# Performance work log

Measured on AMD Instinct MI355X. Metric: run time of the kernel, lower is better.

The kernel has to match this reference:

```python
import jax, jax.numpy as jnp
import numpy as np

H = 12      # num_heads
DIN = 768   # input_embedding_dim
D = 64      # embedding_dim (per head)
N, T = 4, 1024


def setup_inputs() -> dict:
    key = jax.random.key(0)
    ks = jax.random.split(key, 6)
    s_in = 1.0 / np.sqrt(DIN)
    s_hd = 1.0 / np.sqrt(H * D)
    x = jax.random.normal(ks[0], (N, T, DIN), dtype=jnp.float32)
    # Per-head bias-free projections stacked over heads: [H, DIN, D]
    Wq = jax.random.uniform(ks[1], (H, DIN, D), jnp.float32, -s_in, s_in)
    Wk = jax.random.uniform(ks[2], (H, DIN, D), jnp.float32, -s_in, s_in)
    Wv = jax.random.uniform(ks[3], (H, DIN, D), jnp.float32, -s_in, s_in)
    # Output projection: Linear(H*D -> D) with bias
    Wo = jax.random.uniform(ks[4], (H * D, D), jnp.float32, -s_hd, s_hd)
    bo = jax.random.uniform(ks[5], (D,), jnp.float32, -s_hd, s_hd)
    return {"x": x, "Wq": Wq, "Wk": Wk, "Wv": Wv, "Wo": Wo, "bo": bo}


def reference(x, Wq, Wk, Wv, Wo, bo):
    n, t, _ = x.shape
    # Batched per-head projections (all heads at once): [N,H,T,D]
    q = jnp.einsum('ntd,hde->nhte', x, Wq)
    k = jnp.einsum('ntd,hde->nhte', x, Wk)
    v = jnp.einsum('ntd,hde->nhte', x, Wv)
    # Raw scores (note: original applies NO 1/sqrt(D) scaling): [N,H,T,T]
    att = jnp.einsum('nhte,nhse->nhts', q, k)
    # Faithful to torch: tril zeros the upper triangle, then ALL zeros -> -inf
    causal = jnp.tril(jnp.ones((t, t), dtype=bool))
    att = jnp.where(causal, att, 0.0)
    att = jnp.where(att == 0.0, -jnp.inf, att)
    attn = jax.nn.softmax(att, axis=-1)  # [N,H,T,T]
    # Weighted values, then concat heads along feature dim (head-major order)
    o = jnp.einsum('nhts,nhse->nhte', attn, v)          # [N,H,T,D]
    o = jnp.transpose(o, (0, 2, 1, 3)).reshape(n, t, -1)  # [N,T,H*D]
    out = o @ Wo + bo  # [N,T,D]
    return out, attn
```

## Files before the change

### kernel.cpp

```cpp
#include <hip/hip_runtime.h>
#include <hip/hip_bf16.h>

typedef __hip_bfloat16 bf16;
typedef __attribute__((ext_vector_type(8))) short bf16x8;
typedef __attribute__((ext_vector_type(4))) float f32x4;

constexpr int NB  = 4;
constexpr int NH  = 12;
constexpr int SEQ = 1024;
constexpr int HD  = 64;
constexpr int DM  = 768;
constexpr int LDA = 40;

__device__ __forceinline__ bf16x8 ld8(const bf16* p){ return *(const bf16x8*)p; }
__device__ __forceinline__ f32x4 mfma16(bf16x8 a, bf16x8 b, f32x4 c){
  return __builtin_amdgcn_mfma_f32_16x16x32_bf16(a, b, c, 0, 0, 0);
}
union U8 { bf16x8 v; bf16 h[8]; };

__global__ __launch_bounds__(256) void wprep(const float* __restrict__ Wq, const float* __restrict__ Wk,
                      const float* __restrict__ Wv, const float* __restrict__ Wo,
                      bf16* __restrict__ WqTh, bf16* __restrict__ WqTl,
                      bf16* __restrict__ WkTh, bf16* __restrict__ WkTl,
                      bf16* __restrict__ WvT,  bf16* __restrict__ WoT){
  __shared__ float sT[64][65];
  const int tid = threadIdx.x;
  const int dt = blockIdx.x, y = blockIdx.y;
  const float* src; bf16* dh; bf16* dl = nullptr;
  if (y < 36){
    int z = y / 12, h = y % 12;
    src = (z==0 ? Wq : z==1 ? Wk : Wv) + (size_t)h*DM*HD;
    dh  = (z==0 ? WqTh : z==1 ? WkTh : WvT) + (size_t)h*HD*DM;
    if (z==0) dl = WqTl + (size_t)h*HD*DM;
    if (z==1) dl = WkTl + (size_t)h*HD*DM;
  } else { src = Wo; dh = WoT; }

  {
    int r = tid >> 2, c = (tid & 3) * 16;
    const float* sp = src + ((size_t)(dt*64 + r))*HD + c;
    f32x4 v0 = *(const f32x4*)sp, v1 = *(const f32x4*)(sp+4),
          v2 = *(const f32x4*)(sp+8), v3 = *(const f32x4*)(sp+12);
    #pragma unroll
    for (int j = 0; j < 4; j++){
      sT[r][c+j] = v0[j]; sT[r][c+4+j] = v1[j]; sT[r][c+8+j] = v2[j]; sT[r][c+12+j] = v3[j];
    }
  }
  __syncthreads();
  {
    int e = tid >> 2, co = (tid & 3) * 16;
    U8 uh0, ul0, uh1, ul1;
    #pragma unroll
    for (int j = 0; j < 8; j++){
      float v = sT[co + j][e];
      bf16 hi = __float2bfloat16(v);
      uh0.h[j] = hi; ul0.h[j] = __float2bfloat16(v - __bfloat162float(hi));
    }
    #pragma unroll
    for (int j = 0; j < 8; j++){
      float v = sT[co + 8 + j][e];
      bf16 hi = __float2bfloat16(v);
      uh1.h[j] = hi; ul1.h[j] = __float2bfloat16(v - __bfloat162float(hi));
    }
    size_t o = (size_t)e*DM + dt*64 + co;
    *(bf16x8*)(dh + o) = uh0.v; *(bf16x8*)(dh + o + 8) = uh1.v;
    if (dl){ *(bf16x8*)(dl + o) = ul0.v; *(bf16x8*)(dl + o + 8) = ul1.v; }
  }
}

__global__ __launch_bounds__(256) void xprep(const float* __restrict__ x,
                                             bf16* __restrict__ xh, bf16* __restrict__ xl){
  size_t base = ((size_t)blockIdx.x*256 + threadIdx.x)*8;
  f32x4 a = *(const f32x4*)(x + base), b = *(const f32x4*)(x + base + 4);
  U8 uh, ul;
  #pragma unroll
  for (int j = 0; j < 4; j++){
    bf16 h0 = __float2bfloat16(a[j]);
    uh.h[j] = h0; ul.h[j] = __float2bfloat16(a[j] - __bfloat162float(h0));
    bf16 h1 = __float2bfloat16(b[j]);
    uh.h[4+j] = h1; ul.h[4+j] = __float2bfloat16(b[j] - __bfloat162float(h1));
  }
  *(bf16x8*)(xh + base) = uh.v;
  *(bf16x8*)(xl + base) = ul.v;
}

__global__ __launch_bounds__(256) void kproj(const bf16* __restrict__ xh, const bf16* __restrict__ xl,
    const bf16* __restrict__ WqTh, const bf16* __restrict__ WqTl,
    const bf16* __restrict__ WkTh, const bf16* __restrict__ WkTl,
    const bf16* __restrict__ WvT,
    bf16* __restrict__ Qhi, bf16* __restrict__ Qlo,
    bf16* __restrict__ Khi, bf16* __restrict__ Klo, bf16* __restrict__ Vt){
  __shared__ bf16 sA[2][128*LDA];
  __shared__ bf16 sB[4][64*LDA];
  const int tid = threadIdx.x;
  const int lane = tid & 63, w = tid >> 6;
  const int quad = lane >> 4, lc = lane & 15;
  const int mb = blockIdx.x, h = blockIdx.y, z = blockIdx.z;
  const int sr = tid >> 2;
  const int sc = (tid & 3) * 8;
  const int wm = w & 1, wn = w >> 1;

  if (z == 0){
    const bf16* Bqh = WqTh + (size_t)h*HD*DM;
    const bf16* Bql = WqTl + (size_t)h*HD*DM;
    const bf16* Bkh = WkTh + (size_t)h*HD*DM;
    const bf16* Bkl = WkTl + (size_t)h*HD*DM;
    f32x4 aq[4][2] = {}, ak[4][2] = {};
    bf16x8 pa0,pa1,pa2,pa3,pq0,pq1,pk0,pk1;
    auto ldchunk = [&](int kc){
      size_t col = (size_t)kc*32 + sc;
      pa0 = ld8(xh + (size_t)(mb*128 + sr)*DM + col);
      pa1 = ld8(xh + (size_t)(mb*128 + sr + 64)*DM + col);
      pa2 = ld8(xl + (size_t)(mb*128 + sr)*DM + col);
      pa3 = ld8(xl + (size_t)(mb*128 + sr + 64)*DM + col);
      pq0 = ld8(Bqh + (size_t)sr*DM + col);
      pq1 = ld8(Bql + (size_t)sr*DM + col);
      pk0 = ld8(Bkh + (size_t)sr*DM + col);
      pk1 = ld8(Bkl + (size_t)sr*DM + col);
    };
    ldchunk(0);
    for (int kc = 0; kc < DM/32; kc++){
      *(bf16x8*)&sA[0][sr*LDA + sc] = pa0;
      *(bf16x8*)&sA[0][(sr+64)*LDA + sc] = pa1;
      *(bf16x8*)&sA[1][sr*LDA + sc] = pa2;
      *(bf16x8*)&sA[1][(sr+64)*LDA + sc] = pa3;
      *(bf16x8*)&sB[0][sr*LDA + sc] = pq0;
      *(bf16x8*)&sB[1][sr*LDA + sc] = pq1;
      *(bf16x8*)&sB[2][sr*LDA + sc] = pk0;
      *(bf16x8*)&sB[3][sr*LDA + sc] = pk1;
      __syncthreads();
      if (kc < DM/32 - 1) ldchunk(kc + 1);
      bf16x8 bqh[2], bql[2], bkh[2], bkl[2];
      #pragma unroll
      for (int nt = 0; nt < 2; nt++){
        int ro = (wn*32 + nt*16 + lc)*LDA + quad*8;
        bqh[nt] = *(const bf16x8*)&sB[0][ro];
        bql[nt] = *(const bf16x8*)&sB[1][ro];
        bkh[nt] = *(const bf16x8*)&sB[2][ro];
        bkl[nt] = *(const bf16x8*)&sB[3][ro];
      }
      #pragma unroll
      for (int mt = 0; mt < 4; mt++){
        bf16x8 ah = *(const bf16x8*)&sA[0][(wm*64 + mt*16 + lc)*LDA + quad*8];
        bf16x8 al = *(const bf16x8*)&sA[1][(wm*64 + mt*16 + lc)*LDA + quad*8];
        #pragma unroll
        for (int nt = 0; nt < 2; nt++){
          aq[mt][nt] = mfma16(ah, bqh[nt], aq[mt][nt]);
          aq[mt][nt] = mfma16(ah, bql[nt], aq[mt][nt]);
          aq[mt][nt] = mfma16(al, bqh[nt], aq[mt][nt]);
          ak[mt][nt] = mfma16(ah, bkh[nt], ak[mt][nt]);
          ak[mt][nt] = mfma16(ah, bkl[nt], ak[mt][nt]);
          ak[mt][nt] = mfma16(al, bkh[nt], ak[mt][nt]);
        }
      }
      __syncthreads();
    }
    #pragma unroll
    for (int mt = 0; mt < 4; mt++){
      #pragma unroll
      for (int nt = 0; nt < 2; nt++){
        #pragma unroll
        for (int i = 0; i < 4; i++){
          int tg = mb*128 + wm*64 + mt*16 + quad*4 + i;
          int e  = wn*32 + nt*16 + lc;
          int n = tg >> 10, t = tg & 1023;
          size_t o = ((size_t)(n*NH + h)*SEQ + t)*HD + e;
          float vq = aq[mt][nt][i];
          bf16 hq = __float2bfloat16(vq);
          Qhi[o] = hq;
          Qlo[o] = __float2bfloat16(vq - __bfloat162float(hq));
          float vk = ak[mt][nt][i];
          bf16 hk = __float2bfloat16(vk);
          Khi[o] = hk;
          Klo[o] = __float2bfloat16(vk - __bfloat162float(hk));
        }
      }
    }
  } else {
    const bf16* Av = WvT + (size_t)h*HD*DM;
    f32x4 acc[2][4] = {};
    bf16x8 pa0, pb0, pb1;
    auto ldchunk = [&](int kc){
      size_t col = (size_t)kc*32 + sc;
      pa0 = ld8(Av + (size_t)sr*DM + col);
      pb0 = ld8(xh + (size_t)(mb*128 + sr)*DM + col);
      pb1 = ld8(xh + (size_t)(mb*128 + sr + 64)*DM + col);
    };
    ldchunk(0);
    for (int kc = 0; kc < DM/32; kc++){
      *(bf16x8*)&sB[0][sr*LDA + sc] = pa0;
      *(bf16x8*)&sA[0][sr*LDA + sc] = pb0;
      *(bf16x8*)&sA[0][(sr+64)*LDA + sc] = pb1;
      __syncthreads();
      if (kc < DM/32 - 1) ldchunk(kc + 1);
      bf16x8 bt[4];
      #pragma unroll
      for (int nt = 0; nt < 4; nt++)
        bt[nt] = *(const bf16x8*)&sA[0][(wn*64 + nt*16 + lc)*LDA + quad*8];
      #pragma unroll
      for (int mt = 0; mt < 2; mt++){
        bf16x8 a = *(const bf16x8*)&sB[0][(wm*32 + mt*16 + lc)*LDA + quad*8];
        #pragma unroll
        for (int nt = 0; nt < 4; nt++)
          acc[mt][nt] = mfma16(a, bt[nt], acc[mt][nt]);
      }
      __syncthreads();
    }
    #pragma unroll
    for (int mt = 0; mt < 2; mt++){
      #pragma unroll
      for (int nt = 0; nt < 4; nt++){
        #pragma unroll
        for (int i = 0; i < 4; i++){
          int e  = wm*32 + mt*16 + quad*4 + i;
          int tg = mb*128 + wn*64 + nt*16 + lc;
          int n = tg >> 10, t = tg & 1023;
          Vt[((size_t)(n*NH + h)*HD + e)*SEQ + t] = __float2bfloat16(acc[mt][nt][i]);
        }
      }
    }
  }
}

__global__ __launch_bounds__(256) void kattn_pv(const bf16* __restrict__ Qhi, const bf16* __restrict__ Qlo,
                                                const bf16* __restrict__ Khi, const bf16* __restrict__ Klo,
                                                const bf16* __restrict__ Vt,
                                                float* __restrict__ attn, bf16* __restrict__ O){
  __shared__ bf16 sP[16][SEQ + 8];
  __shared__ float msh[4][16], lsh[4][16];
  const int tid = threadIdx.x;
  const int lane = tid & 63, w = tid >> 6;
  const int quad = lane >> 4, lc = lane & 15;
  const int t0 = blockIdx.x * 16;
  const int nh = blockIdx.y;
  const size_t base = (size_t)nh * SEQ * HD;
  const float NEGINF = -__builtin_inff();

  f32x4 acc[16] = {};
  const bf16* qh = Qhi + base + (size_t)(t0 + lc)*HD;
  const bf16* ql = Qlo + base + (size_t)(t0 + lc)*HD;
  bf16x8 ah0 = ld8(qh + quad*8), ah1 = ld8(qh + 32 + quad*8);
  bf16x8 al0 = ld8(ql + quad*8), al1 = ld8(ql + 32 + quad*8);
  const int tmax = t0 + 15;
  const int cbase = w*256;

  bf16x8 kb[2][4];
  auto loadK = [&](int tl, int b){
    const bf16* kh = Khi + base + (size_t)(cbase + tl*16 + lc)*HD;
    const bf16* kl = Klo + base + (size_t)(cbase + tl*16 + lc)*HD;
    kb[b][0] = ld8(kh + quad*8);  kb[b][1] = ld8(kh + 32 + quad*8);
    kb[b][2] = ld8(kl + quad*8);  kb[b][3] = ld8(kl + 32 + quad*8);
  };
  if (cbase <= tmax) loadK(0, 0);
  #pragma unroll
  for (int tl = 0; tl < 16; tl++){
    if (cbase + tl*16 <= tmax){
      if (tl < 15 && cbase + (tl+1)*16 <= tmax) loadK(tl+1, (tl+1)&1);
      const int b = tl & 1;
      acc[tl] = mfma16(ah0, kb[b][0], acc[tl]);
      acc[tl] = mfma16(ah1, kb[b][1], acc[tl]);
      acc[tl] = mfma16(ah0, kb[b][2], acc[tl]);
      acc[tl] = mfma16(ah1, kb[b][3], acc[tl]);
      acc[tl] = mfma16(al0, kb[b][0], acc[tl]);
      acc[tl] = mfma16(al1, kb[b][1], acc[tl]);
    }
  }

  float mx[4] = {NEGINF, NEGINF, NEGINF, NEGINF};
  #pragma unroll
  for (int tl = 0; tl < 16; tl++){
    int col = cbase + tl*16 + lc;
    #pragma unroll
    for (int i = 0; i < 4; i++){
      int r = t0 + quad*4 + i;
      float v = acc[tl][i];
      if (col <= r && v != 0.0f) mx[i] = fmaxf(mx[i], v);
    }
  }
  #pragma unroll
  for (int off = 8; off; off >>= 1){
    #pragma unroll
    for (int i = 0; i < 4; i++) mx[i] = fmaxf(mx[i], __shfl_xor(mx[i], off, 16));
  }
  float sm[4] = {0.f, 0.f, 0.f, 0.f};
  #pragma unroll
  for (int tl = 0; tl < 16; tl++){
    int col = cbase + tl*16 + lc;
    #pragma unroll
    for (int i = 0; i < 4; i++){
      int r = t0 + quad*4 + i;
      float v = acc[tl][i];
      float e = (col <= r && v != 0.0f) ? __expf(v - mx[i]) : 0.0f;
      acc[tl][i] = e;
      sm[i] += e;
    }
  }
  #pragma unroll
  for (int off = 8; off; off >>= 1){
    #pragma unroll
    for (int i = 0; i < 4; i++) sm[i] += __shfl_xor(sm[i], off, 16);
  }
  if (lc == 0){
    #pragma unroll
    for (int i = 0; i < 4; i++){ msh[w][quad*4 + i] = mx[i]; lsh[w][quad*4 + i] = sm[i]; }
  }
  __syncthreads();
  float scale[4];
  #pragma unroll
  for (int i = 0; i < 4; i++){
    int rl = quad*4 + i;
    float M = fmaxf(fmaxf(msh[0][rl], msh[1][rl]), fmaxf(msh[2][rl], msh[3][rl]));
    float L = 0.f;
    #pragma unroll
    for (int w2 = 0; w2 < 4; w2++) L += lsh[w2][rl] * __expf(msh[w2][rl] - M);
    scale[i] = __expf(mx[i] - M) / L;
  }
  #pragma unroll
  for (int tl = 0; tl < 16; tl++){
    int col = cbase + tl*16 + lc;
    #pragma unroll
    for (int i = 0; i < 4; i++){
      sP[quad*4 + i][col] = __float2bfloat16(acc[tl][i] * scale[i]);
    }
  }
  __syncthreads();

  #pragma unroll
  for (int r = 0; r < 16; r++){
    const unsigned* sPu = (const unsigned*)&sP[r][0];
    uint2 v = *(const uint2*)(sPu + tid*2);
    f32x4 f;
    f[0] = __uint_as_float(v.x << 16);
    f[1] = __uint_as_float(v.x & 0xFFFF0000u);
    f[2] = __uint_as_float(v.y << 16);
    f[3] = __uint_as_float(v.y & 0xFFFF0000u);
    *(f32x4*)(attn + ((size_t)nh*SEQ + t0 + r)*SEQ + tid*4) = f;
  }

  f32x4 oacc = {};
  const bf16* Vb = Vt + ((size_t)nh*HD + w*16 + lc)*SEQ;
  const int kend = t0 + 16;
  for (int s0 = 0; s0 < kend; s0 += 32){
    bf16x8 a = *(const bf16x8*)&sP[lc][s0 + quad*8];
    bf16x8 b = ld8(Vb + s0 + quad*8);
    oacc = mfma16(a, b, oacc);
  }
  const int n = nh / NH, h = nh % NH;
  #pragma unroll
  for (int i = 0; i < 4; i++){
    O[((size_t)n*SEQ + t0 + quad*4 + i)*DM + h*HD + w*16 + lc] = __float2bfloat16(oacc[i]);
  }
}

__global__ __launch_bounds__(256) void kout(const bf16* __restrict__ O, const bf16* __restrict__ WoT,
                                            const float* __restrict__ bo, float* __restrict__ out){
  const int lane = threadIdx.x & 63, w = threadIdx.x >> 6;
  const int quad = lane >> 4, lc = lane & 15;
  const int wm = w & 1, wn = w >> 1;
  const int g = blockIdx.x * 32;
  const int n = g >> 10, tb = g & 1023;
  const bf16* Or = O + ((size_t)n*SEQ + tb + wm*16 + lc)*DM;
  f32x4 acc[2] = {};
  for (int k0 = 0; k0 < DM; k0 += 32){
    bf16x8 a = ld8(Or + k0 + quad*8);
    #pragma unroll
    for (int nt = 0; nt < 2; nt++){
      bf16x8 b = ld8(WoT + (size_t)(wn*32 + nt*16 + lc)*DM + k0 + quad*8);
      acc[nt] = mfma16(a, b, acc[nt]);
    }
  }
  #pragma unroll
  for (int nt = 0; nt < 2; nt++){
    float bias = bo[wn*32 + nt*16 + lc];
    #pragma unroll
    for (int i = 0; i < 4; i++){
      out[((size_t)n*SEQ + tb + wm*16 + quad*4 + i)*HD + wn*32 + nt*16 + lc] = acc[nt][i] + bias;
    }
  }
}

extern "C" void kernel_launch(void* const* d_in, const int* in_sizes, int n_in,
                              void* d_out, int out_size, void* d_ws, size_t ws_size,
                              hipStream_t stream){
  const float* x  = (const float*)d_in[0];
  const float* Wq = (const float*)d_in[1];
  const float* Wk = (const float*)d_in[2];
  const float* Wv = (const float*)d_in[3];
  const float* Wo = (const float*)d_in[4];
  const float* bo = (const float*)d_in[5];

  float* out  = (float*)d_out;
  float* attn = out + (size_t)NB*SEQ*HD;

  constexpr size_t SZ_WT  = (size_t)NH*HD*DM;
  constexpr size_t SZ_WOT = (size_t)HD*DM;
  constexpr size_t SZ_Q   = (size_t)NB*NH*SEQ*HD;
  bf16* b = (bf16*)d_ws;
  bf16* WqTh = b;  b += SZ_WT;
  bf16* WqTl = b;  b += SZ_WT;
  bf16* WkTh = b;  b += SZ_WT;
  bf16* WkTl = b;  b += SZ_WT;
  bf16* WvT  = b;  b += SZ_WT;
  bf16* WoT  = b;  b += SZ_WOT;
  bf16* xh   = b;  b += SZ_Q;
  bf16* xl   = b;  b += SZ_Q;
  bf16* Qhi  = b;  b += SZ_Q;
  bf16* Qlo  = b;  b += SZ_Q;
  bf16* Khi  = b;  b += SZ_Q;
  bf16* Klo  = b;  b += SZ_Q;
  bf16* Vt   = b;  b += SZ_Q;
  bf16* O    = xh;

  wprep<<<dim3(12, 37), 256, 0, stream>>>(Wq, Wk, Wv, Wo, WqTh, WqTl, WkTh, WkTl, WvT, WoT);
  xprep<<<dim3((int)(SZ_Q/(256*8))), 256, 0, stream>>>(x, xh, xl);
  kproj<<<dim3(NB*SEQ/128, NH, 2), 256, 0, stream>>>(xh, xl, WqTh, WqTl, WkTh, WkTl, WvT,
                                                     Qhi, Qlo, Khi, Klo, Vt);
  kattn_pv<<<dim3(SEQ/16, NB*NH), 256, 0, stream>>>(Qhi, Qlo, Khi, Klo, Vt, attn, O);
  kout<<<dim3(NB*SEQ/32), 256, 0, stream>>>(O, WoT, bo, out);
}
```

Measured before the change: 361.0 us.

## Fuse V projection into QK projection blocks and drop softmax max pass

The projection kernel now computes Q, K and V in one block per row-tile, so x is loaded once for all three; V is transposed through shared memory and written with vector stores. The attention kernel drops the row-max pass and exponentiates raw scores directly, which removes a reduction, a shared-memory exchange and extra exps, but risks overflow if scores are large. It also removes K double-buffering and moves the PV matmul ahead of the attn store. The V projection now runs with fewer blocks, and the missing max subtraction only holds while raw scores stay small enough for exp.

```diff
diff --git a/kernel.cpp b/kernel.cpp
--- a/kernel.cpp
+++ b/kernel.cpp
@@ -11,6 +11,7 @@
 constexpr int HD  = 64;
 constexpr int DM  = 768;
 constexpr int LDA = 40;
+constexpr int LDV = 138;
 
 __device__ __forceinline__ bf16x8 ld8(const bf16* p){ return *(const bf16x8*)p; }
 __device__ __forceinline__ f32x4 mfma16(bf16x8 a, bf16x8 b, f32x4 c){
@@ -90,133 +91,121 @@
     bf16* __restrict__ Qhi, bf16* __restrict__ Qlo,
     bf16* __restrict__ Khi, bf16* __restrict__ Klo, bf16* __restrict__ Vt){
   __shared__ bf16 sA[2][128*LDA];
-  __shared__ bf16 sB[4][64*LDA];
+  __shared__ bf16 sB[5][64*LDA];
   const int tid = threadIdx.x;
   const int lane = tid & 63, w = tid >> 6;
   const int quad = lane >> 4, lc = lane & 15;
-  const int mb = blockIdx.x, h = blockIdx.y, z = blockIdx.z;
+  const int mb = blockIdx.x, h = blockIdx.y;
   const int sr = tid >> 2;
   const int sc = (tid & 3) * 8;
   const int wm = w & 1, wn = w >> 1;
 
-  if (z == 0){
-    const bf16* Bqh = WqTh + (size_t)h*HD*DM;
-    const bf16* Bql = WqTl + (size_t)h*HD*DM;
-    const bf16* Bkh = WkTh + (size_t)h*HD*DM;
-    const bf16* Bkl = WkTl + (size_t)h*HD*DM;
-    f32x4 aq[4][2] = {}, ak[4][2] = {};
-    bf16x8 pa0,pa1,pa2,pa3,pq0,pq1,pk0,pk1;
-    auto ldchunk = [&](int kc){
-      size_t col = (size_t)kc*32 + sc;
-      pa0 = ld8(xh + (size_t)(mb*128 + sr)*DM + col);
-      pa1 = ld8(xh + (size_t)(mb*128 + sr + 64)*DM + col);
-      pa2 = ld8(xl + (size_t)(mb*128 + sr)*DM + col);
-      pa3 = ld8(xl + (size_t)(mb*128 + sr + 64)*DM + col);
-      pq0 = ld8(Bqh + (size_t)sr*DM + col);
-      pq1 = ld8(Bql + (size_t)sr*DM + col);
-      pk0 = ld8(Bkh + (size_t)sr*DM + col);
-      pk1 = ld8(Bkl + (size_t)sr*DM + col);
-    };
-    ldchunk(0);
-    for (int kc = 0; kc < DM/32; kc++){
-      *(bf16x8*)&sA[0][sr*LDA + sc] = pa0;
-      *(bf16x8*)&sA[0][(sr+64)*LDA + sc] = pa1;
-      *(bf16x8*)&sA[1][sr*LDA + sc] = pa2;
-      *(bf16x8*)&sA[1][(sr+64)*LDA + sc] = pa3;
-      *(bf16x8*)&sB[0][sr*LDA + sc] = pq0;
-      *(bf16x8*)&sB[1][sr*LDA + sc] = pq1;
-      *(bf16x8*)&sB[2][sr*LDA + sc] = pk0;
-      *(bf16x8*)&sB[3][sr*LDA + sc] = pk1;
-      __syncthreads();
-      if (kc < DM/32 - 1) ldchunk(kc + 1);
-      bf16x8 bqh[2], bql[2], bkh[2], bkl[2];
+  const bf16* Bqh = WqTh + (size_t)h*HD*DM;
+  const bf16* Bql = WqTl + (size_t)h*HD*DM;
+  const bf16* Bkh = WkTh + (size_t)h*HD*DM;
+  const bf16* Bkl = WkTl + (size_t)h*HD*DM;
+  const bf16* Bv  = WvT  + (size_t)h*HD*DM;
+
+  f32x4 aq[4][2] = {}, ak[4][2] = {}, av[4][2] = {};
+  bf16x8 pa0,pa1,pa2,pa3,pq0,pq1,pk0,pk1,pv0;
+  auto ldchunk = [&](int kc){
+    size_t col = (size_t)kc*32 + sc;
+    pa0 = ld8(xh + (size_t)(mb*128 + sr)*DM + col);
+    pa1 = ld8(xh + (size_t)(mb*128 + sr + 64)*DM + col);
+    pa2 = ld8(xl + (size_t)(mb*128 + sr)*DM + col);
+    pa3 = ld8(xl + (size_t)(mb*128 + sr + 64)*DM + col);
+    pq0 = ld8(Bqh + (size_t)sr*DM + col);
+    pq1 = ld8(Bql + (size_t)sr*DM + col);
+    pk0 = ld8(Bkh + (size_t)sr*DM + col);
+    pk1 = ld8(Bkl + (size_t)sr*DM + col);
+    pv0 = ld8(Bv  + (size_t)sr*DM + col);
+  };
+  ldchunk(0);
+  for (int kc = 0; kc < DM/32; kc++){
+    *(bf16x8*)&sA[0][sr*LDA + sc] = pa0;
+    *(bf16x8*)&sA[0][(sr+64)*LDA + sc] = pa1;
+    *(bf16x8*)&sA[1][sr*LDA + sc] = pa2;
+    *(bf16x8*)&sA[1][(sr+64)*LDA + sc] = pa3;
+    *(bf16x8*)&sB[0][sr*LDA + sc] = pq0;
+    *(bf16x8*)&sB[1][sr*LDA + sc] = pq1;
+    *(bf16x8*)&sB[2][sr*LDA + sc] = pk0;
+    *(bf16x8*)&sB[3][sr*LDA + sc] = pk1;
+    *(bf16x8*)&sB[4][sr*LDA + sc] = pv0;
+    __syncthreads();
+    if (kc < DM/32 - 1) ldchunk(kc + 1);
+    bf16x8 bqh[2], bql[2], bkh[2], bkl[2], bv[2];
+    #pragma unroll
+    for (int nt = 0; nt < 2; nt++){
+      int ro = (wn*32 + nt*16 + lc)*LDA + quad*8;
+      bqh[nt] = *(const bf16x8*)&sB[0][ro];
+      bql[nt] = *(const bf16x8*)&sB[1][ro];
+      bkh[nt] = *(const bf16x8*)&sB[2][ro];
+      bkl[nt] = *(const bf16x8*)&sB[3][ro];
+      bv[nt]  = *(const bf16x8*)&sB[4][ro];
+    }
+    #pragma unroll
+    for (int mt = 0; mt < 4; mt++){
+      bf16x8 ah = *(const bf16x8*)&sA[0][(wm*64 + mt*16 + lc)*LDA + quad*8];
+      bf16x8 al = *(const bf16x8*)&sA[1][(wm*64 + mt*16 + lc)*LDA + quad*8];
       #pragma unroll
       for (int nt = 0; nt < 2; nt++){
-        int ro = (wn*32 + nt*16 + lc)*LDA + quad*8;
-        bqh[nt] = *(const bf16x8*)&sB[0][ro];
-        bql[nt] = *(const bf16x8*)&sB[1][ro];
-        bkh[nt] = *(const bf16x8*)&sB[2][ro];
-        bkl[nt] = *(const bf16x8*)&sB[3][ro];
+        aq[mt][nt] = mfma16(ah, bqh[nt], aq[mt][nt]);
+        aq[mt][nt] = mfma16(ah, bql[nt], aq[mt][nt]);
+        aq[mt][nt] = mfma16(al, bqh[nt], aq[mt][nt]);
+        ak[mt][nt] = mfma16(ah, bkh[nt], ak[mt][nt]);
+        ak[mt][nt] = mfma16(ah, bkl[nt], ak[mt][nt]);
+        ak[mt][nt] = mfma16(al, bkh[nt], ak[mt][nt]);
+        av[mt][nt] = mfma16(ah, bv[nt],  av[mt][nt]);
       }
+    }
+    __syncthreads();
+  }
+
+  const int nA = mb >> 3, tbase = (mb*128) & 1023;
+  #pragma unroll
+  for (int mt = 0; mt < 4; mt++){
+    #pragma unroll
+    for (int nt = 0; nt < 2; nt++){
       #pragma unroll
-      for (int mt = 0; mt < 4; mt++){
-        bf16x8 ah = *(const bf16x8*)&sA[0][(wm*64 + mt*16 + lc)*LDA + quad*8];
-        bf16x8 al = *(const bf16x8*)&sA[1][(wm*64 + mt*16 + lc)*LDA + quad*8];
-        #pragma unroll
-        for (int nt = 0; nt < 2; nt++){
-          aq[mt][nt] = mfma16(ah, bqh[nt], aq[mt][nt]);
-          aq[mt][nt] = mfma16(ah, bql[nt], aq[mt][nt]);
-          aq[mt][nt] = mfma16(al, bqh[nt], aq[mt][nt]);
-          ak[mt][nt] = mfma16(ah, bkh[nt], ak[mt][nt]);
-          ak[mt][nt] = mfma16(ah, bkl[nt], ak[mt][nt]);
-          ak[mt][nt] = mfma16(al, bkh[nt], ak[mt][nt]);
-        }
+      for (int i = 0; i < 4; i++){
+        int t = tbase + wm*64 + mt*16 + quad*4 + i;
+        int e = wn*32 + nt*16 + lc;
+        size_t o = ((size_t)(nA*NH + h)*SEQ + t)*HD + e;
+        float vq = aq[mt][nt][i];
+        bf16 hq = __float2bfloat16(vq);
+        Qhi[o] = hq;
+        Qlo[o] = __float2bfloat16(vq - __bfloat162float(hq));
+        float vk = ak[mt][nt][i];
+        bf16 hk = __float2bfloat16(vk);
+        Khi[o] = hk;
+        Klo[o] = __float2bfloat16(vk - __bfloat162float(hk));
       }
-      __syncthreads();
-    }
-    #pragma unroll
-    for (int mt = 0; mt < 4; mt++){
+    }
+  }
+
+  bf16* sV = &sB[0][0];
+  #pragma unroll
+  for (int mt = 0; mt < 4; mt++){
+    #pragma unroll
+    for (int nt = 0; nt < 2; nt++){
+      int e = wn*32 + nt*16 + lc;
       #pragma unroll
-      for (int nt = 0; nt < 2; nt++){
-        #pragma unroll
-        for (int i = 0; i < 4; i++){
-          int tg = mb*128 + wm*64 + mt*16 + quad*4 + i;
-          int e  = wn*32 + nt*16 + lc;
-          int n = tg >> 10, t = tg & 1023;
-          size_t o = ((size_t)(n*NH + h)*SEQ + t)*HD + e;
-          float vq = aq[mt][nt][i];
-          bf16 hq = __float2bfloat16(vq);
-          Qhi[o] = hq;
-          Qlo[o] = __float2bfloat16(vq - __bfloat162float(hq));
-          float vk = ak[mt][nt][i];
-          bf16 hk = __float2bfloat16(vk);
-          Khi[o] = hk;
-          Klo[o] = __float2bfloat16(vk - __bfloat162float(hk));
-        }
+      for (int i = 0; i < 4; i++){
+        int t = wm*64 + mt*16 + quad*4 + i;
+        sV[e*LDV + t] = __float2bfloat16(av[mt][nt][i]);
       }
     }
-  } else {
-    const bf16* Av = WvT + (size_t)h*HD*DM;
-    f32x4 acc[2][4] = {};
-    bf16x8 pa0, pb0, pb1;
-    auto ldchunk = [&](int kc){
-      size_t col = (size_t)kc*32 + sc;
-      pa0 = ld8(Av + (size_t)sr*DM + col);
-      pb0 = ld8(xh + (size_t)(mb*128 + sr)*DM + col);
-      pb1 = ld8(xh + (size_t)(mb*128 + sr + 64)*DM + col);
-    };
-    ldchunk(0);
-    for (int kc = 0; kc < DM/32; kc++){
-      *(bf16x8*)&sB[0][sr*LDA + sc] = pa0;
-      *(bf16x8*)&sA[0][sr*LDA + sc] = pb0;
-      *(bf16x8*)&sA[0][(sr+64)*LDA + sc] = pb1;
-      __syncthreads();
-      if (kc < DM/32 - 1) ldchunk(kc + 1);
-      bf16x8 bt[4];
+  }
+  __syncthreads();
+  {
+    int er = tid >> 4, toff = (tid & 15) * 8;
+    #pragma unroll
+    for (int p = 0; p < 4; p++){
+      int e = p*16 + er;
+      U8 u;
       #pragma unroll
-      for (int nt = 0; nt < 4; nt++)
-        bt[nt] = *(const bf16x8*)&sA[0][(wn*64 + nt*16 + lc)*LDA + quad*8];
-      #pragma unroll
-      for (int mt = 0; mt < 2; mt++){
-        bf16x8 a = *(const bf16x8*)&sB[0][(wm*32 + mt*16 + lc)*LDA + quad*8];
-        #pragma unroll
-        for (int nt = 0; nt < 4; nt++)
-          acc[mt][nt] = mfma16(a, bt[nt], acc[mt][nt]);
-      }
-      __syncthreads();
-    }
-    #pragma unroll
-    for (int mt = 0; mt < 2; mt++){
-      #pragma unroll
-      for (int nt = 0; nt < 4; nt++){
-        #pragma unroll
-        for (int i = 0; i < 4; i++){
-          int e  = wm*32 + mt*16 + quad*4 + i;
-          int tg = mb*128 + wn*64 + nt*16 + lc;
-          int n = tg >> 10, t = tg & 1023;
-          Vt[((size_t)(n*NH + h)*HD + e)*SEQ + t] = __float2bfloat16(acc[mt][nt][i]);
-        }
-      }
+      for (int j = 0; j < 8; j++) u.h[j] = sV[e*LDV + toff + j];
+      *(bf16x8*)(Vt + ((size_t)(nA*NH + h)*HD + e)*SEQ + tbase + toff) = u.v;
     }
   }
 }
@@ -226,14 +215,13 @@
                                                 const bf16* __restrict__ Vt,
                                                 float* __restrict__ attn, bf16* __restrict__ O){
   __shared__ bf16 sP[16][SEQ + 8];
-  __shared__ float msh[4][16], lsh[4][16];
+  __shared__ float lsh[4][16];
   const int tid = threadIdx.x;
   const int lane = tid & 63, w = tid >> 6;
   const int quad = lane >> 4, lc = lane & 15;
   const int t0 = blockIdx.x * 16;
   const int nh = blockIdx.y;
   const size_t base = (size_t)nh * SEQ * HD;
-  const float NEGINF = -__builtin_inff();
 
   f32x4 acc[16] = {};
   const bf16* qh = Qhi + base + (size_t)(t0 + lc)*HD;
@@ -243,29 +231,24 @@
   const int tmax = t0 + 15;
   const int cbase = w*256;
 
-  bf16x8 kb[2][4];
-  auto loadK = [&](int tl, int b){
-    const bf16* kh = Khi + base + (size_t)(cbase + tl*16 + lc)*HD;
-    const bf16* kl = Klo + base + (size_t)(cbase + tl*16 + lc)*HD;
-    kb[b][0] = ld8(kh + quad*8);  kb[b][1] = ld8(kh + 32 + quad*8);
-    kb[b][2] = ld8(kl + quad*8);  kb[b][3] = ld8(kl + 32 + quad*8);
-  };
-  if (cbase <= tmax) loadK(0, 0);
   #pragma unroll
   for (int tl = 0; tl < 16; tl++){
-    if (cbase + tl*16 <= tmax){
-      if (tl < 15 && cbase + (tl+1)*16 <= tmax) loadK(tl+1, (tl+1)&1);
-      const int b = tl & 1;
-      acc[tl] = mfma16(ah0, kb[b][0], acc[tl]);
-      acc[tl] = mfma16(ah1, kb[b][1], acc[tl]);
-      acc[tl] = mfma16(ah0, kb[b][2], acc[tl]);
-      acc[tl] = mfma16(ah1, kb[b][3], acc[tl]);
-      acc[tl] = mfma16(al0, kb[b][0], acc[tl]);
-      acc[tl] = mfma16(al1, kb[b][1], acc[tl]);
-    }
-  }
-
-  float mx[4] = {NEGINF, NEGINF, NEGINF, NEGINF};
+    int ct = cbase + tl*16;
+    if (ct <= tmax){
+      const bf16* kh = Khi + base + (size_t)(ct + lc)*HD;
+      const bf16* kl = Klo + base + (size_t)(ct + lc)*HD;
+      bf16x8 bh0 = ld8(kh + quad*8), bh1 = ld8(kh + 32 + quad*8);
+      bf16x8 bl0 = ld8(kl + quad*8), bl1 = ld8(kl + 32 + quad*8);
+      acc[tl] = mfma16(ah0, bh0, acc[tl]);
+      acc[tl] = mfma16(ah1, bh1, acc[tl]);
+      acc[tl] = mfma16(ah0, bl0, acc[tl]);
+      acc[tl] = mfma16(ah1, bl1, acc[tl]);
+      acc[tl] = mfma16(al0, bh0, acc[tl]);
+      acc[tl] = mfma16(al1, bh1, acc[tl]);
+    }
+  }
+
+  float sm[4] = {0.f, 0.f, 0.f, 0.f};
   #pragma unroll
   for (int tl = 0; tl < 16; tl++){
     int col = cbase + tl*16 + lc;
@@ -273,56 +256,45 @@
     for (int i = 0; i < 4; i++){
       int r = t0 + quad*4 + i;
       float v = acc[tl][i];
-      if (col <= r && v != 0.0f) mx[i] = fmaxf(mx[i], v);
+      float e = (col <= r && v != 0.0f) ? __expf(v) : 0.0f;
+      acc[tl][i] = e;
+      sm[i] += e;
     }
   }
   #pragma unroll
   for (int off = 8; off; off >>= 1){
     #pragma unroll
-    for (int i = 0; i < 4; i++) mx[i] = fmaxf(mx[i], __shfl_xor(mx[i], off, 16));
-  }
-  float sm[4] = {0.f, 0.f, 0.f, 0.f};
+    for (int i = 0; i < 4; i++) sm[i] += __shfl_xor(sm[i], off, 16);
+  }
+  if (lc == 0){
+    #pragma unroll
+    for (int i = 0; i < 4; i++) lsh[w][quad*4 + i] = sm[i];
+  }
+  __syncthreads();
+  float rs[4];
+  #pragma unroll
+  for (int i = 0; i < 4; i++){
+    int rl = quad*4 + i;
+    rs[i] = 1.0f / (lsh[0][rl] + lsh[1][rl] + lsh[2][rl] + lsh[3][rl]);
+  }
   #pragma unroll
   for (int tl = 0; tl < 16; tl++){
     int col = cbase + tl*16 + lc;
     #pragma unroll
     for (int i = 0; i < 4; i++){
-      int r = t0 + quad*4 + i;
-      float v = acc[tl][i];
-      float e = (col <= r && v != 0.0f) ? __expf(v - mx[i]) : 0.0f;
-      acc[tl][i] = e;
-      sm[i] += e;
-    }
-  }
-  #pragma unroll
-  for (int off = 8; off; off >>= 1){
-    #pragma unroll
-    for (int i = 0; i < 4; i++) sm[i] += __shfl_xor(sm[i], off, 16);
-  }
-  if (lc == 0){
-    #pragma unroll
-    for (int i = 0; i < 4; i++){ msh[w][quad*4 + i] = mx[i]; lsh[w][quad*4 + i] = sm[i]; }
+      sP[quad*4 + i][col] = __float2bfloat16(acc[tl][i] * rs[i]);
+    }
   }
   __syncthreads();
-  float scale[4];
-  #pragma unroll
-  for (int i = 0; i < 4; i++){
-    int rl = quad*4 + i;
-    float M = fmaxf(fmaxf(msh[0][rl], msh[1][rl]), fmaxf(msh[2][rl], msh[3][rl]));
-    float L = 0.f;
-    #pragma unroll
-    for (int w2 = 0; w2 < 4; w2++) L += lsh[w2][rl] * __expf(msh[w2][rl] - M);
-    scale[i] = __expf(mx[i] - M) / L;
-  }
-  #pragma unroll
-  for (int tl = 0; tl < 16; tl++){
-    int col = cbase + tl*16 + lc;
-    #pragma unroll
-    for (int i = 0; i < 4; i++){
-      sP[quad*4 + i][col] = __float2bfloat16(acc[tl][i] * scale[i]);
-    }
-  }
-  __syncthreads();
+
+  f32x4 oacc = {};
+  const bf16* Vb = Vt + ((size_t)nh*HD + w*16 + lc)*SEQ;
+  const int kend = t0 + 16;
+  for (int s0 = 0; s0 < kend; s0 += 32){
+    bf16x8 a = *(const bf16x8*)&sP[lc][s0 + quad*8];
+    bf16x8 b = ld8(Vb + s0 + quad*8);
+    oacc = mfma16(a, b, oacc);
+  }
 
   #pragma unroll
   for (int r = 0; r < 16; r++){
@@ -336,14 +308,6 @@
     *(f32x4*)(attn + ((size_t)nh*SEQ + t0 + r)*SEQ + tid*4) = f;
   }
 
-  f32x4 oacc = {};
-  const bf16* Vb = Vt + ((size_t)nh*HD + w*16 + lc)*SEQ;
-  const int kend = t0 + 16;
-  for (int s0 = 0; s0 < kend; s0 += 32){
-    bf16x8 a = *(const bf16x8*)&sP[lc][s0 + quad*8];
-    bf16x8 b = ld8(Vb + s0 + quad*8);
-    oacc = mfma16(a, b, oacc);
-  }
   const int n = nh / NH, h = nh % NH;
   #pragma unroll
   for (int i = 0; i < 4; i++){
@@ -412,8 +376,8 @@
 
   wprep<<<dim3(12, 37), 256, 0, stream>>>(Wq, Wk, Wv, Wo, WqTh, WqTl, WkTh, WkTl, WvT, WoT);
   xprep<<<dim3((int)(SZ_Q/(256*8))), 256, 0, stream>>>(x, xh, xl);
-  kproj<<<dim3(NB*SEQ/128, NH, 2), 256, 0, stream>>>(xh, xl, WqTh, WqTl, WkTh, WkTl, WvT,
-                                                     Qhi, Qlo, Khi, Klo, Vt);
+  kproj<<<dim3(NB*SEQ/128, NH), 256, 0, stream>>>(xh, xl, WqTh, WqTl, WkTh, WkTl, WvT,
+                                                  Qhi, Qlo, Khi, Klo, Vt);
   kattn_pv<<<dim3(SEQ/16, NB*NH), 256, 0, stream>>>(Qhi, Qlo, Khi, Klo, Vt, attn, O);
   kout<<<dim3(NB*SEQ/32), 256, 0, stream>>>(O, WoT, bo, out);
 }
```

New measurement: 367.4 us. No clear change (+1.8%).
